# Optimization experiments

Measured on AMD Instinct MI355X. Metric: run time of the kernel, lower is better.

The kernel has to match this reference:

```python
import jax, jax.numpy as jnp
import numpy as np

B, T, N = 16, 16, 1024          # patients, max visits, code_num
C, G, H, A, P = 48, 32, 150, 32, 32  # code_size, graph_size, hidden_size, t_attention_size, pool attn size
OUT = 1
NEG = -1e30


def setup_inputs() -> dict:
    key = jax.random.key(0)
    ks = jax.random.split(key, 20)
    code_x = (jax.random.uniform(ks[0], (B, T, N)) < 0.2).astype(jnp.float32)
    neighbors = (jax.random.uniform(ks[1], (B, T, N)) < 0.2).astype(jnp.float32)
    cat = jax.random.randint(ks[2], (B, T, N), 0, 8)
    # divided[..., 0/1/2] = disjoint m1 (persistent) / m2 (emerging-neighbor) / m3 (emerging-unrelated) masks
    divided = jnp.stack([(cat == 0), (cat == 1), (cat == 2)], axis=-1).astype(jnp.int32)
    lens = jax.random.randint(ks[3], (B,), 1, T + 1)
    prior = jax.random.uniform(ks[4], (N,))
    adj = (jax.random.uniform(ks[5], (N, N)) * (jax.random.uniform(ks[6], (N, N)) < 0.05)).astype(jnp.float32)

    def nrm(k, shape, scale=0.05):
        return (jax.random.normal(k, shape) * scale).astype(jnp.float32)

    return dict(
        code_x=code_x, divided=divided, neighbors=neighbors, lens=lens, prior=prior, adj=adj,
        c_emb=nrm(ks[7], (N, C)), n_emb=nrm(ks[8], (N, C)), u_emb=nrm(ks[9], (N, G)),
        Wg=nrm(ks[10], (C, G)), bg=jnp.zeros((G,), jnp.float32),
        W_ih=nrm(ks[11], (3 * H, G)), b_ih=jnp.zeros((3 * H,), jnp.float32),
        W_hh=nrm(ks[12], (3 * H, H)), b_hh=jnp.zeros((3 * H,), jnp.float32),
        Wq=nrm(ks[13], (G, A)), bq=jnp.zeros((A,), jnp.float32),
        Wk=nrm(ks[14], (G, A)), bk=jnp.zeros((A,), jnp.float32),
        Wv=nrm(ks[15], (G, H)), bv=jnp.zeros((H,), jnp.float32),
        Wp=nrm(ks[16], (H, P)), bp=jnp.zeros((P,), jnp.float32),
        ctx=nrm(ks[17], (P,)),
        Wc=nrm(ks[18], (H, OUT)), bc=jnp.zeros((OUT,), jnp.float32),
    )


def _forward(code_x, divided, neighbors, lens, prior, adj, c_emb, n_emb, u_emb,
             Wg, bg, W_ih, b_ih, W_hh, b_hh, Wq, bq, Wk, bk, Wv, bv,
             Wp, bp, ctx, Wc, bc):
    pr = prior[:, None]                                  # [N,1] disease prior scaling of graph messages
    scale = 1.0 / jnp.sqrt(jnp.asarray(A, jnp.float32))

    def gru(x, h):
        # torch nn.GRUCell semantics; x: [B,N,G], h: [B,N,H]
        gi = jnp.einsum('bng,kg->bnk', x, W_ih) + b_ih
        gh = jnp.einsum('bnh,kh->bnk', h, W_hh) + b_hh
        ir, iz, i_n = jnp.split(gi, 3, -1)
        hr, hz, h_n = jnp.split(gh, 3, -1)
        r = jax.nn.sigmoid(ir + hr)
        z = jax.nn.sigmoid(iz + hz)
        cand = jnp.tanh(i_n + r * h_n)
        return (1.0 - z) * cand + z * h

    def step(carry, xs):
        h_prev, no_prev, t = carry
        cx, nb, dv = xs                                  # [B,N], [B,N], [B,N,3]
        c = cx[..., None]
        n = nb[..., None]
        # --- GraphLayer: adjacency message passing, prior-weighted ---
        ce = c * c_emb                                   # [B,N,C]
        ne = n * n_emb
        agg_c = jnp.einsum('mn,bnc->bmc', adj, ce) * pr
        agg_n = jnp.einsum('mn,bnc->bmc', adj, ne) * pr
        co = jax.nn.leaky_relu((ce + c * (agg_c + agg_n)) @ Wg + bg)   # [B,N,G]
        no = jax.nn.leaky_relu((ne + n * (agg_n + agg_c)) @ Wg + bg)
        # --- TransitionLayer ---
        m1 = dv[..., 0] > 0
        m2 = dv[..., 1] > 0
        m3 = dv[..., 2] > 0
        m23 = m2 | m3
        h_gru = gru(co, h_prev)                          # GRU branch for persistent codes (m1)
        # attention branch: queries = prev-step neighbor embeddings (m2) or unrelated embeddings (m3)
        qf = jnp.where(m2[..., None], no_prev, 0.0) + jnp.where(m3[..., None], u_emb, 0.0)
        q = qf @ Wq + bq
        k = co @ Wk + bk
        v = co @ Wv + bv                                 # [B,N,H]
        g = jnp.einsum('bma,bna->bmn', q, k) * scale     # scores over active m2|m3 keys only
        g = jnp.where(m23[:, None, :], g, NEG)
        h_att = jnp.tanh(jnp.einsum('bmn,bnh->bmh', jax.nn.softmax(g, axis=-1), v))
        t_pos = (t > 0).astype(co.dtype)                 # m23 branch only runs for t > 0 (as in original)
        h_new = jnp.where(m1[..., None], h_gru, 0.0) + t_pos * jnp.where(m23[..., None], h_att, 0.0)
        # masked maxes (0 when the index set is empty, as in original)
        om1 = jnp.max(jnp.where(m1[..., None], h_gru, NEG), axis=1)
        om1 = jnp.where(jnp.any(m1, axis=1)[:, None], om1, 0.0)
        om23 = jnp.max(jnp.where(m23[..., None], h_att, NEG), axis=1)
        om23 = jnp.where(jnp.any(m23, axis=1)[:, None], om23, 0.0)
        out_t = om1 + t_pos * om23                       # [B,H]
        return (h_new, no, t + 1), out_t

    h0 = jnp.zeros((B, N, H), jnp.float32)
    no0 = jnp.zeros((B, N, G), jnp.float32)
    xs = (jnp.transpose(code_x, (1, 0, 2)),
          jnp.transpose(neighbors, (1, 0, 2)),
          jnp.transpose(divided, (1, 0, 2, 3)))
    _, outs = jax.lax.scan(step, (h0, no0, jnp.int32(0)), xs)
    outs = jnp.transpose(outs, (1, 0, 2))                # [B,T,H]
    # --- DotProductAttention pooling over valid (ragged) timesteps ---
    vu = (outs @ Wp + bp) @ ctx                          # [B,T]
    valid = jnp.arange(T)[None, :] < lens[:, None]
    score = jax.nn.softmax(jnp.where(valid, vu, NEG), axis=-1)
    pooled = jnp.sum(outs * score[..., None], axis=1)    # [B,H]
    # --- Classifier (dropout identity at eval, activation=None) ---
    return pooled @ Wc + bc


def reference(code_x, divided, neighbors, lens, prior, adj, c_emb, n_emb, u_emb,
              Wg, bg, W_ih, b_ih, W_hh, b_hh, Wq, bq, Wk, bk, Wv, bv,
              Wp, bp, ctx, Wc, bc):
    return _forward(code_x, divided, neighbors, lens, prior, adj, c_emb, n_emb, u_emb,
                    Wg, bg, W_ih, b_ih, W_hh, b_hh, Wq, bq, Wk, bk, Wv, bv,
                    Wp, bp, ctx, Wc, bc)
```

## Files before the change

kernel.cpp:

```cpp
#include <hip/hip_runtime.h>

#define B_ 16
#define T_ 16
#define N_ 1024
#define C_ 48
#define G_ 32
#define H_ 150
#define A_ 32
#define P_ 32
#define H3_ 450
#define NNZ_CAP 262144
#define CAP1 256
#define CAP23 384
#define CHCAP 40960
#define CHCAPL 16384
#define SCALE_ 0.17677669529663687f

__device__ __forceinline__ unsigned fenc(float f){
  unsigned u = __float_as_uint(f);
  return (u & 0x80000000u) ? ~u : (u | 0x80000000u);
}
__device__ __forceinline__ float fdec(unsigned e){
  unsigned u = (e & 0x80000000u) ? (e & 0x7fffffffu) : ~e;
  return __uint_as_float(u);
}
__device__ __forceinline__ float sigmf(float x){ return 1.f/(1.f+__expf(-x)); }
__device__ __forceinline__ float wmaxf(float v){
  #pragma unroll
  for (int d=32; d>0; d>>=1) v = fmaxf(v, __shfl_xor(v,d));
  return v;
}

#define FMA16(W, PTR, ACC) do { \
    const float4* _c4 = (const float4*)(PTR); \
    float4 _c0=_c4[0], _c1=_c4[1], _c2=_c4[2], _c3=_c4[3]; \
    ACC[0]=fmaf((W),_c0.x,ACC[0]); ACC[1]=fmaf((W),_c0.y,ACC[1]); \
    ACC[2]=fmaf((W),_c0.z,ACC[2]); ACC[3]=fmaf((W),_c0.w,ACC[3]); \
    ACC[4]=fmaf((W),_c1.x,ACC[4]); ACC[5]=fmaf((W),_c1.y,ACC[5]); \
    ACC[6]=fmaf((W),_c1.z,ACC[6]); ACC[7]=fmaf((W),_c1.w,ACC[7]); \
    ACC[8]=fmaf((W),_c2.x,ACC[8]); ACC[9]=fmaf((W),_c2.y,ACC[9]); \
    ACC[10]=fmaf((W),_c2.z,ACC[10]); ACC[11]=fmaf((W),_c2.w,ACC[11]); \
    ACC[12]=fmaf((W),_c3.x,ACC[12]); ACC[13]=fmaf((W),_c3.y,ACC[13]); \
    ACC[14]=fmaf((W),_c3.z,ACC[14]); ACC[15]=fmaf((W),_c3.w,ACC[15]); \
  } while(0)

__global__ void k_csr_cnt(const float* __restrict__ adj, int* __restrict__ rcnt){
  int m = blockIdx.x; int tid = threadIdx.x;
  int c = 0;
  for (int n = tid; n < N_; n += 256) c += (adj[(size_t)m*N_+n] != 0.f) ? 1 : 0;
  __shared__ int sr[256];
  sr[tid]=c; __syncthreads();
  for (int s=128; s>0; s>>=1){ if (tid<s) sr[tid]+=sr[tid+s]; __syncthreads(); }
  if (tid==0) rcnt[m]=sr[0];
}
__global__ void k_csr_scan(const int* __restrict__ rcnt, int* __restrict__ rowptr){
  int lane = threadIdx.x;
  int s = 0;
  for (int r=0;r<16;++r) s += rcnt[lane*16+r];
  int incl = s;
  for (int d=1; d<64; d<<=1){ int y = __shfl_up(incl, d); if (lane>=d) incl += y; }
  int run = incl - s;
  for (int r=0;r<16;++r){ rowptr[lane*16+r] = run; run += rcnt[lane*16+r]; }
  if (lane==63) rowptr[N_] = incl;
}
__global__ void k_csr_fill(const float* __restrict__ adj, const float* __restrict__ prior,
                           const int* __restrict__ rowptr,
                           int* __restrict__ ccol, float* __restrict__ cval){
  int m = blockIdx.x; int lane = threadIdx.x;
  int base = rowptr[m];
  float pm = prior[m];
  for (int it=0; it<N_/64; ++it){
    int n = it*64+lane;
    float a = adj[(size_t)m*N_+n];
    bool pnz = (a != 0.f);
    unsigned long long mk = __ballot(pnz);
    if (pnz){
      int idx = base + __popcll(mk & ((1ULL<<lane)-1ULL));
      if (idx < NNZ_CAP){ ccol[idx]=n; cval[idx]=a*pm; }
    }
    base += __popcll(mk);
  }
}

__global__ void k_masks(const int* __restrict__ divided, int* __restrict__ lst23,
                        int* __restrict__ pos1,
                        int* __restrict__ cnt23, int* __restrict__ cnt1){
  int bt = blockIdx.x; int lane = threadIdx.x;
  int base23=0, base1=0;
  for (int it=0; it<N_/64; ++it){
    int n = it*64+lane;
    const int* dv = &divided[((size_t)bt*N_+n)*3];
    int d0=dv[0], d1=dv[1], d2=dv[2];
    bool p23 = (d1>0)||(d2>0); bool p1 = d0>0;
    unsigned long long mk23 = __ballot(p23);
    unsigned long long mk1  = __ballot(p1);
    unsigned long long ltm = (1ULL<<lane)-1ULL;
    if (p23){ int idx = base23 + __popcll(mk23 & ltm); lst23[(size_t)bt*N_+idx]=n; }
    if (p1){ int idx = base1 + __popcll(mk1 & ltm); pos1[(size_t)bt*N_+n]=idx; }
    base23 += __popcll(mk23); base1 += __popcll(mk1);
  }
  if (lane==0){ cnt23[bt]=base23; cnt1[bt]=base1; }
}

__global__ void k_chains(const int* __restrict__ divided,
                         unsigned* __restrict__ chN, int* __restrict__ nchN,
                         unsigned* __restrict__ chH, int* __restrict__ nchH,
                         unsigned* __restrict__ chL, int* __restrict__ nchL){
  int idx = blockIdx.x*256 + threadIdx.x;
  if (idx >= B_*N_) return;
  int b = idx >> 10, n = idx & (N_-1);
  unsigned m1m = 0;
  for (int t=0;t<T_;++t){
    int d0 = divided[(((size_t)(b*T_+t))*N_ + n)*3];
    if (d0>0) m1m |= (1u<<t);
  }
  unsigned heads = m1m & ~(m1m<<1);
  while (heads){
    int t0 = __builtin_ctz(heads); heads &= (heads-1u);
    unsigned run = m1m >> t0;
    int len = __builtin_ctz(~run);
    unsigned enc = ((unsigned)b<<18)|((unsigned)n<<8)|((unsigned)t0<<4)|(unsigned)(len-1);
    int f = 0;
    if (t0 >= 2){
      size_t pidx = ((size_t)(b*T_+t0-1)*N_ + n)*3;
      if ((divided[pidx+1] | divided[pidx+2]) > 0) f = 1;
    }
    if (f){ int i2 = atomicAdd(nchH,1); if (i2 < CHCAP) chH[i2]=enc; }
    else  { int i2 = atomicAdd(nchN,1); if (i2 < CHCAP) chN[i2]=enc; }
    if (len >= 2){
      int i2 = atomicAdd(nchL, 1);
      if (i2 < CHCAPL) chL[i2] = enc;
    }
  }
}

__global__ void k_wt(const float* __restrict__ W_ih, const float* __restrict__ W_hh,
                     const float* __restrict__ Wq, const float* __restrict__ bq,
                     const float* __restrict__ Wk, const float* __restrict__ Wv,
                     float* __restrict__ WihT, float* __restrict__ WhhT,
                     float* __restrict__ Md, float* __restrict__ WvT){
  int idx = blockIdx.x*256+threadIdx.x;
  if (idx < G_*H3_){ int g=idx/H3_, k=idx-g*H3_; WihT[g*H3_+k]=W_ih[(size_t)k*G_+g]; }
  int idx2 = idx - G_*H3_;
  if (idx2>=0 && idx2 < H_*H3_){ int h=idx2/H3_, k=idx2-h*H3_; WhhT[h*H3_+k]=W_hh[(size_t)k*H_+h]; }
  int e = idx - (G_*H3_ + H_*H3_);
  if (e>=0 && e<1024){
    int g=e>>5, gp=e&31;
    float acc=0.f;
    #pragma unroll
    for (int a=0;a<A_;++a) acc = fmaf(Wq[g*A_+a], Wk[gp*A_+a], acc);
    Md[e]=acc;
  }
  int e2 = e - 1024;
  if (e2>=0 && e2<32){
    float acc=0.f;
    #pragma unroll
    for (int a=0;a<A_;++a) acc = fmaf(Wk[e2*A_+a], bq[a], acc);
    Md[1024+e2]=acc;
  }
  int e3 = e - 1056;
  if (e3>=0 && e3 < H_*G_){
    int h = e3>>5, g = e3&31;
    WvT[e3] = Wv[(size_t)g*H_+h];
  }
}

__global__ void k_init(float* __restrict__ om23f, int* __restrict__ nchN,
                       int* __restrict__ nchH, int* __restrict__ nchL){
  int i = blockIdx.x*256+threadIdx.x;
  if (i<B_*T_*H_){ om23f[i]=0.f; }
  if (i==0){ *nchN = 0; *nchH = 0; *nchL = 0; }
}

__global__ __launch_bounds__(256) void k_cono(
    const float* __restrict__ code_x, const float* __restrict__ neighbors,
    const int* __restrict__ divided,
    const int* __restrict__ rowptr, const int* __restrict__ ccol, const float* __restrict__ cval,
    const float* __restrict__ c_emb, const float* __restrict__ n_emb,
    const float* __restrict__ Wg, const float* __restrict__ bg,
    float* __restrict__ co, float* __restrict__ no_)
{
  __shared__ float sCo[4][C_], sNo[4][C_];
  int w = threadIdx.x >> 6, lane = threadIdx.x & 63;
  int gw = blockIdx.x*4 + w;
  int bt = gw >> 10, m = gw & (N_-1);
  int t = bt & (T_-1);
  const int* dv = &divided[(size_t)gw*3];
  int d0=dv[0], d1=dv[1], d2=dv[2];
  bool needCo = (d0|d1|d2) > 0;
  bool needNo = (t < T_-1) && (divided[((size_t)(gw+N_))*3+1] > 0);
  if (!needCo && !needNo) return;
  float cxm = code_x[gw], nbm = neighbors[gw];
  float acc = 0.f;
  bool needAcc = (needCo && cxm!=0.f) || (needNo && nbm!=0.f);
  if (needAcc){
    int s = rowptr[m], e = rowptr[m+1];
    if (s > NNZ_CAP) s = NNZ_CAP;
    if (e > NNZ_CAP) e = NNZ_CAP;
    int btN = bt << 10;
    for (int base = s; base < e; base += 64){
      int j = base + lane;
      int cc = 0; float wx = 0.f, wy = 0.f;
      if (j < e){
        cc = ccol[j];
        float cv = cval[j];
        float xs = code_x[btN+cc], ys = neighbors[btN+cc];
        wx = cv*xs; wy = cv*ys;
      }
      unsigned long long mk = __ballot(wx!=0.f || wy!=0.f);
      while (mk){
        int u0 = __builtin_ctzll(mk); mk &= (mk-1ULL);
        int u1 = -1;
        if (mk){ u1 = __builtin_ctzll(mk); mk &= (mk-1ULL); }
        int u1s = (u1>=0)? u1 : u0;
        int n0 = __shfl(cc,u0); float a0x=__shfl(wx,u0), a0y=__shfl(wy,u0);
        int n1 = __shfl(cc,u1s); float a1x=__shfl(wx,u1s), a1y=__shfl(wy,u1s);
        float ce0=0.f,ne0=0.f,ce1=0.f,ne1=0.f;
        if (lane < C_){
          ce0 = c_emb[(size_t)n0*C_+lane]; ne0 = n_emb[(size_t)n0*C_+lane];
          ce1 = c_emb[(size_t)n1*C_+lane]; ne1 = n_emb[(size_t)n1*C_+lane];
        }
        acc = fmaf(a0x, ce0, acc); acc = fmaf(a0y, ne0, acc);
        if (u1>=0){ acc = fmaf(a1x, ce1, acc); acc = fmaf(a1y, ne1, acc); }
      }
    }
  }
  if (lane < C_){
    sCo[w][lane] = cxm * (c_emb[(size_t)m*C_+lane] + acc);
    sNo[w][lane] = nbm * (n_emb[(size_t)m*C_+lane] + acc);
  }
  asm volatile("s_waitcnt lgkmcnt(0)" ::: "memory");
  int g = lane & 31; bool isNo = lane >= 32;
  const float* src = isNo ? sNo[w] : sCo[w];
  float a2 = bg[g];
  #pragma unroll
  for (int c=0;c<C_;++c) a2 = fmaf(src[c], Wg[c*G_+g], a2);
  float r = a2 >= 0.f ? a2 : 0.01f*a2;
  if (isNo ? needNo : needCo){
    float* dst = isNo ? no_ : co;
    dst[(size_t)gw*G_ + g] = r;
  }
}

__global__ __launch_bounds__(768) void k_attn(
    const float* __restrict__ co, const float* __restrict__ no_,
    const float* __restrict__ u_emb, const int* __restrict__ divided,
    const int* __restrict__ lst23, const int* __restrict__ cnt23, const int* __restrict__ pos1,
    const float* __restrict__ Md, const float* __restrict__ WvT, const float* __restrict__ bv,
    float* __restrict__ hsel, float* __restrict__ om23f)
{
  int b = blockIdx.x; int t = blockIdx.y + 1; int bt = b*T_ + t;
  int cnt = cnt23[bt]; if (cnt > CAP23) cnt = CAP23;
  if (cnt == 0) return;
  __shared__ int   sLst[CAP23];
  __shared__ __align__(16) float sCo[CAP23][G_];
  __shared__ float sL[CAP23];
  __shared__ unsigned sMax[H_];
  int tid = threadIdx.x;
  int grp = (tid >= 384) ? 1 : 0;
  int r   = tid - 384*grp;
  unsigned sent = fenc(-1e30f);
  for (int i=tid; i<cnt; i+=768) sLst[i] = lst23[(size_t)bt*N_+i];
  for (int i=tid; i<H_; i+=768) sMax[i] = sent;
  __syncthreads();
  for (int i=tid; i<cnt*8; i+=768){
    int rrow = i>>3, seg = i&7;
    float4 v = *(const float4*)&co[((((size_t)bt<<10) + sLst[rrow])<<5) + seg*4];
    *(float4*)&sCo[rrow][seg*4] = v;
  }
  bool act = (r < cnt);
  int n = 0;
  float qpp[G_];
  if (act){
    n = sLst[r];
    int d1 = divided[((size_t)bt*N_+n)*3+1];
    const float* qsrc = (d1>0) ? &no_[((((size_t)(bt-1))<<10)+n)<<5] : &u_emb[(size_t)n*G_];
    float4 qv[8];
    #pragma unroll
    for (int j=0;j<8;++j) qv[j] = ((const float4*)qsrc)[j];
    #pragma unroll
    for (int j=0;j<G_;++j) qpp[j] = Md[1024+j];
    #pragma unroll
    for (int g=0; g<G_; ++g){
      float qfg = (g&3)==0 ? qv[g>>2].x : (g&3)==1 ? qv[g>>2].y : (g&3)==2 ? qv[g>>2].z : qv[g>>2].w;
      const float4* mr = (const float4*)&Md[g*G_];
      #pragma unroll
      for (int j=0;j<8;++j){
        float4 mj = mr[j];
        qpp[4*j+0] = fmaf(qfg, mj.x, qpp[4*j+0]);
        qpp[4*j+1] = fmaf(qfg, mj.y, qpp[4*j+1]);
        qpp[4*j+2] = fmaf(qfg, mj.z, qpp[4*j+2]);
        qpp[4*j+3] = fmaf(qfg, mj.w, qpp[4*j+3]);
      }
    }
  } else {
    #pragma unroll
    for (int j=0;j<G_;++j) qpp[j]=0.f;
  }
  __syncthreads();
  int half = (cnt+1)>>1;
  int c0 = grp ? half : 0;
  int c1 = grp ? cnt  : half;
  float pbar[G_]; float l = 0.f;
  #pragma unroll
  for (int j=0;j<G_;++j) pbar[j]=0.f;
  if (act){
    #pragma unroll 2
    for (int c=c0;c<c1;++c){
      const float4* col = (const float4*)&sCo[c][0];
      float4 xv[8];
      #pragma unroll
      for (int j=0;j<8;++j) xv[j]=col[j];
      float d0=0.f,d1v=0.f,d2v=0.f,d3=0.f;
      #pragma unroll
      for (int j=0;j<8;j+=4){
        d0 = fmaf(qpp[4*j+0], xv[j].x, d0); d1v = fmaf(qpp[4*j+1], xv[j].y, d1v);
        d2v = fmaf(qpp[4*j+2], xv[j].z, d2v); d3 = fmaf(qpp[4*j+3], xv[j].w, d3);
        d0 = fmaf(qpp[4*j+4], xv[j+1].x, d0); d1v = fmaf(qpp[4*j+5], xv[j+1].y, d1v);
        d2v = fmaf(qpp[4*j+6], xv[j+1].z, d2v); d3 = fmaf(qpp[4*j+7], xv[j+1].w, d3);
        d0 = fmaf(qpp[4*j+8], xv[j+2].x, d0); d1v = fmaf(qpp[4*j+9], xv[j+2].y, d1v);
        d2v = fmaf(qpp[4*j+10], xv[j+2].z, d2v); d3 = fmaf(qpp[4*j+11], xv[j+2].w, d3);
        d0 = fmaf(qpp[4*j+12], xv[j+3].x, d0); d1v = fmaf(qpp[4*j+13], xv[j+3].y, d1v);
        d2v = fmaf(qpp[4*j+14], xv[j+3].z, d2v); d3 = fmaf(qpp[4*j+15], xv[j+3].w, d3);
      }
      float dot = (d0+d1v)+(d2v+d3);
      float pv = __expf(dot*SCALE_);
      l += pv;
      #pragma unroll
      for (int j=0;j<8;++j){
        pbar[4*j+0] = fmaf(pv, xv[j].x, pbar[4*j+0]);
        pbar[4*j+1] = fmaf(pv, xv[j].y, pbar[4*j+1]);
        pbar[4*j+2] = fmaf(pv, xv[j].z, pbar[4*j+2]);
        pbar[4*j+3] = fmaf(pv, xv[j].w, pbar[4*j+3]);
      }
    }
  }
  __syncthreads();
  if (act && grp==0){
    #pragma unroll
    for (int j=0;j<G_;++j) sCo[r][j] = pbar[j];
    sL[r] = l;
  }
  __syncthreads();
  if (act && grp==1){
    #pragma unroll
    for (int j=0;j<G_;++j) sCo[r][j] += pbar[j];
    sL[r] += l;
  }
  __syncthreads();
  float pb[G_];
  if (act){
    float inv = 1.f / sL[r];
    const float4* pr = (const float4*)&sCo[r][0];
    #pragma unroll
    for (int j=0;j<8;++j){
      float4 pv4 = pr[j];
      pb[4*j+0]=pv4.x*inv; pb[4*j+1]=pv4.y*inv; pb[4*j+2]=pv4.z*inv; pb[4*j+3]=pv4.w*inv;
    }
  } else {
    #pragma unroll
    for (int j=0;j<G_;++j) pb[j]=0.f;
  }
  bool wsel=false; float* hd=nullptr;
  if (act && t+1 < T_){
    size_t nidx = ((size_t)b*T_+(t+1))*N_ + n;
    if (divided[nidx*3+0] > 0){
      int pos = pos1[nidx];
      if (pos >= 0 && pos < CAP1){ wsel=true; hd=&hsel[(((size_t)b*T_+t)*CAP1 + pos)*H_]; }
    }
  }
  int lane = tid & 63;
  int hA = grp*75, hB = hA + 75;
  for (int h=hA; h<hB; ++h){
    float acc = bv[h];
    const float4* wr = (const float4*)&WvT[h*G_];
    #pragma unroll
    for (int j=0;j<8;++j){
      float4 wj = wr[j];
      acc = fmaf(pb[4*j+0], wj.x, acc);
      acc = fmaf(pb[4*j+1], wj.y, acc);
      acc = fmaf(pb[4*j+2], wj.z, acc);
      acc = fmaf(pb[4*j+3], wj.w, acc);
    }
    float o = act ? tanhf(acc) : -1e30f;
    float om = wmaxf(o);
    if (lane==0) atomicMax(&sMax[h], fenc(om));
    if (wsel) hd[h] = o;
  }
  __syncthreads();
  for (int i=tid; i<H_; i+=768) om23f[(size_t)bt*H_+i] = fdec(sMax[i]);
}

__global__ __launch_bounds__(256) void k_gruheadN(
    const float* __restrict__ co, const int* __restrict__ pos1,
    const unsigned* __restrict__ chN, const int* __restrict__ nchN,
    const float* __restrict__ WihT, const float* __restrict__ b_ih,
    const float* __restrict__ b_hh, float* __restrict__ gout)
{
  __shared__ __align__(16) float sCoT[G_][16];
  __shared__ float sG[16][452];
  __shared__ int sBt[16], sN[16], sPos[16];
  int tid = threadIdx.x;
  int NC = *nchN; if (NC > CHCAP) NC = CHCAP;
  int base = blockIdx.x * 16;
  if (base >= NC) return;
  int num = min(16, NC - base);
  if (tid < 16){
    if (tid < num){
      unsigned cl = chN[base+tid];
      int b = cl>>18, n = (cl>>8)&1023, t0 = (cl>>4)&15;
      int bt = b*T_ + t0;
      sBt[tid]=bt; sN[tid]=n; sPos[tid]=pos1[(size_t)bt*N_+n];
    } else { sBt[tid]=0; sN[tid]=0; sPos[tid]=-1; }
  }
  __syncthreads();
  for (int i=tid; i<G_*16; i+=256){
    int g = i>>4, ii = i&15;
    sCoT[g][ii] = (ii<num) ? co[((size_t)sBt[ii]*N_+sN[ii])*G_+g] : 0.f;
  }
  __syncthreads();
  for (int pass=0; pass<2; ++pass){
    int k = pass*256 + tid;
    if (k < H3_){
      float acc[16];
      #pragma unroll
      for (int u=0;u<16;++u) acc[u]=0.f;
      for (int g=0; g<G_; ++g){
        float wih = WihT[g*H3_ + k];
        FMA16(wih, &sCoT[g][0], acc);
      }
      #pragma unroll
      for (int u=0;u<16;++u) sG[u][k] = acc[u];
    }
  }
  __syncthreads();
  for (int i=tid; i<num*152; i+=256){
    int s = i/152, h = i - s*152;
    if (h < H_){
      int pos = sPos[s];
      if (pos >= 0 && pos < CAP1){
        float r = sigmf(sG[s][h]       + b_ih[h]       + b_hh[h]);
        float z = sigmf(sG[s][h+H_]    + b_ih[h+H_]    + b_hh[h+H_]);
        float cand = tanhf(sG[s][h+2*H_] + b_ih[h+2*H_] + r*b_hh[h+2*H_]);
        gout[((size_t)sBt[s]*CAP1 + pos)*H_ + h] = (1.f-z)*cand;
      }
    }
  }
}

__global__ __launch_bounds__(256) void k_gruheadH(
    const float* __restrict__ co, const float* __restrict__ hsel,
    const int* __restrict__ pos1,
    const unsigned* __restrict__ chH, const int* __restrict__ nchH,
    const float* __restrict__ WihT, const float* __restrict__ b_ih,
    const float* __restrict__ WhhT, const float* __restrict__ b_hh,
    float* __restrict__ gout)
{
  __shared__ __align__(16) float sCoT[G_][16];
  __shared__ __align__(16) float sHT[152][16];
  __shared__ float sG[16][452];
  __shared__ float sGhn[16][152];
  __shared__ int sBt[16], sN[16], sPos[16], sHo[16];
  int tid = threadIdx.x;
  int NC = *nchH; if (NC > CHCAP) NC = CHCAP;
  int base = blockIdx.x * 16;
  if (base >= NC) return;
  int num = min(16, NC - base);
  if (tid < 16){
    if (tid < num){
      unsigned cl = chH[base+tid];
      int b = cl>>18, n = (cl>>8)&1023, t0 = (cl>>4)&15;
      int bt = b*T_ + t0;
      int pos = pos1[(size_t)bt*N_+n];
      sBt[tid]=bt; sN[tid]=n; sPos[tid]=pos;
      sHo[tid] = (b*T_ + (t0-1))*CAP1 + ((pos>=0 && pos<CAP1) ? pos : 0);
    } else { sBt[tid]=0; sN[tid]=0; sPos[tid]=-1; sHo[tid]=0; }
  }
  __syncthreads();
  for (int i=tid; i<G_*16; i+=256){
    int g = i>>4, ii = i&15;
    sCoT[g][ii] = (ii<num) ? co[((size_t)sBt[ii]*N_+sN[ii])*G_+g] : 0.f;
  }
  for (int i=tid; i<152*16; i+=256){
    int q = i>>4, ii = i&15;
    float v = 0.f;
    if (ii < num && q < H_) v = hsel[(size_t)sHo[ii]*H_ + q];
    sHT[q][ii] = v;
  }
  __syncthreads();
  for (int pass=0; pass<2; ++pass){
    int k = pass*256 + tid;
    if (k < H3_){
      float acc[16];
      #pragma unroll
      for (int u=0;u<16;++u) acc[u]=0.f;
      for (int g=0; g<G_; ++g){
        float wih = WihT[g*H3_ + k];
        FMA16(wih, &sCoT[g][0], acc);
      }
      #pragma unroll
      for (int u=0;u<16;++u) sG[u][k] = acc[u];
    }
  }
  for (int pass=0; pass<2; ++pass){
    int k = pass*256 + tid;
    if (k < H3_){
      float acc[16];
      #pragma unroll
      for (int u=0;u<16;++u) acc[u]=0.f;
      for (int q=0; q<H_; ++q){
        float whh = WhhT[q*H3_ + k];
        FMA16(whh, &sHT[q][0], acc);
      }
      if (k < 2*H_){
        #pragma unroll
        for (int u=0;u<16;++u) sG[u][k] += acc[u];
      } else {
        #pragma unroll
        for (int u=0;u<16;++u) sGhn[u][k-2*H_] = acc[u];
      }
    }
  }
  __syncthreads();
  for (int i=tid; i<num*152; i+=256){
    int s = i/152, h = i - s*152;
    if (h < H_){
      int pos = sPos[s];
      if (pos >= 0 && pos < CAP1){
        float hv = sHT[h][s];
        float r = sigmf(sG[s][h]       + b_ih[h]       + b_hh[h]);
        float z = sigmf(sG[s][h+H_]    + b_ih[h+H_]    + b_hh[h+H_]);
        float cand = tanhf(sG[s][h+2*H_] + b_ih[h+2*H_] + r*(sGhn[s][h] + b_hh[h+2*H_]));
        float o = (1.f-z)*cand + z*hv;
        gout[((size_t)sBt[s]*CAP1 + pos)*H_ + h] = o;
      }
    }
  }
}

__global__ __launch_bounds__(256) void k_grutail(
    const float* __restrict__ co, const int* __restrict__ pos1,
    const unsigned* __restrict__ chainsL, const int* __restrict__ nchL,
    const float* __restrict__ WihT, const float* __restrict__ b_ih,
    const float* __restrict__ WhhT, const float* __restrict__ b_hh,
    float* __restrict__ gout)
{
  __shared__ float hst[4][4][H_];
  int w = threadIdx.x >> 6, lane = threadIdx.x & 63;
  int NC = *nchL; if (NC > CHCAPL) NC = CHCAPL;
  int cbase = (blockIdx.x*4 + w)*4;
  if (cbase >= NC) return;

  int cbv[4], cnv[4], t0v[4], lenv[4];
  #pragma unroll
  for (int u=0;u<4;++u){
    int cid = cbase+u; bool ca = cid < NC;
    unsigned cl = chainsL[ca ? cid : (NC-1)];
    cbv[u]=cl>>18; cnv[u]=(cl>>8)&1023; t0v[u]=(cl>>4)&15;
    lenv[u]= ca ? (int)((cl&15)+1) : 1;
  }
  int maxlen = lenv[0];
  #pragma unroll
  for (int u=1;u<4;++u) maxlen = max(maxlen, lenv[u]);

  int h0=lane,h1=lane+64,h2=lane+128; bool has2=(h2<H_); int h2c=has2?h2:0;
  float bi[9], bh[9];
  bi[0]=b_ih[h0]; bi[1]=b_ih[h0+H_]; bi[2]=b_ih[h0+2*H_];
  bi[3]=b_ih[h1]; bi[4]=b_ih[h1+H_]; bi[5]=b_ih[h1+2*H_];
  bi[6]=b_ih[h2c]; bi[7]=b_ih[h2c+H_]; bi[8]=b_ih[h2c+2*H_];
  bh[0]=b_hh[h0]; bh[1]=b_hh[h0+H_]; bh[2]=b_hh[h0+2*H_];
  bh[3]=b_hh[h1]; bh[4]=b_hh[h1+H_]; bh[5]=b_hh[h1+2*H_];
  bh[6]=b_hh[h2c]; bh[7]=b_hh[h2c+H_]; bh[8]=b_hh[h2c+2*H_];

  for (int s=1; s<maxlen; ++s){
    bool as[4]; int btv[4];
    const float* hp[4];
    #pragma unroll
    for (int u=0;u<4;++u){
      as[u] = s < lenv[u];
      int t = t0v[u] + (as[u] ? s : 0);
      btv[u] = cbv[u]*T_ + t;
      if (s == 1 && as[u]){
        int btp = btv[u] - 1;
        int posp = pos1[(size_t)btp*N_ + cnv[u]];
        if (posp < 0 || posp >= CAP1) posp = 0;
        hp[u] = &gout[((size_t)btp*CAP1 + posp)*H_];
      } else {
        hp[u] = &hst[w][u][0];
      }
    }
    float gi[4][9], gh[4][9];
    #pragma unroll
    for (int u=0;u<4;++u){
      #pragma unroll
      for (int j=0;j<9;++j){ gi[u][j]=bi[j]; gh[u][j]=bh[j]; }
    }
    const float* cop[4];
    #pragma unroll
    for (int u=0;u<4;++u) cop[u] = &co[((size_t)btv[u]*N_ + cnv[u])*G_];
    for (int g=0; g<G_; ++g){
      const float* wr = &WihT[g*H3_];
      float wv[9];
      wv[0]=wr[h0]; wv[1]=wr[h0+H_]; wv[2]=wr[h0+2*H_];
      wv[3]=wr[h1]; wv[4]=wr[h1+H_]; wv[5]=wr[h1+2*H_];
      wv[6]=wr[h2c]; wv[7]=wr[h2c+H_]; wv[8]=wr[h2c+2*H_];
      #pragma unroll
      for (int u=0;u<4;++u){
        float cg = cop[u][g];
        #pragma unroll
        for (int j=0;j<9;++j) gi[u][j]=fmaf(cg, wv[j], gi[u][j]);
      }
    }
    for (int q=0;q<H_;++q){
      const float* wr=&WhhT[q*H3_];
      float wv[9];
      wv[0]=wr[h0]; wv[1]=wr[h0+H_]; wv[2]=wr[h0+2*H_];
      wv[3]=wr[h1]; wv[4]=wr[h1+H_]; wv[5]=wr[h1+2*H_];
      wv[6]=wr[h2c]; wv[7]=wr[h2c+H_]; wv[8]=wr[h2c+2*H_];
      #pragma unroll
      for (int u=0;u<4;++u){
        float hv = hp[u][q];
        #pragma unroll
        for (int j=0;j<9;++j) gh[u][j]=fmaf(hv, wv[j], gh[u][j]);
      }
    }
    #pragma unroll
    for (int u=0;u<4;++u){
      if (as[u]){
        float hv0 = hp[u][h0];
        float hv1 = hp[u][h1];
        float hv2 = has2 ? hp[u][h2] : 0.f;
        float r0=sigmf(gi[u][0]+gh[u][0]), z0=sigmf(gi[u][1]+gh[u][1]);
        float cd0=tanhf(gi[u][2]+r0*gh[u][2]);
        float o0=(1.f-z0)*cd0 + z0*hv0;
        float r1=sigmf(gi[u][3]+gh[u][3]), z1=sigmf(gi[u][4]+gh[u][4]);
        float cd1=tanhf(gi[u][5]+r1*gh[u][5]);
        float o1=(1.f-z1)*cd1 + z1*hv1;
        float o2=0.f;
        if (has2){
          float r2=sigmf(gi[u][6]+gh[u][6]), z2=sigmf(gi[u][7]+gh[u][7]);
          float cd2=tanhf(gi[u][8]+r2*gh[u][8]);
          o2=(1.f-z2)*cd2 + z2*hv2;
        }
        float* hd = &hst[w][u][0];
        hd[h0]=o0; hd[h1]=o1; if (has2) hd[h2]=o2;
        int pos = pos1[(size_t)btv[u]*N_ + cnv[u]];
        if (pos >= 0 && pos < CAP1){
          float* gd = &gout[((size_t)btv[u]*CAP1 + pos)*H_];
          gd[h0]=o0; gd[h1]=o1; if (has2) gd[h2]=o2;
        }
      }
    }
    asm volatile("s_waitcnt lgkmcnt(0)" ::: "memory");
  }
}

__global__ __launch_bounds__(256) void k_om1(
    const float* __restrict__ gout, const int* __restrict__ cnt1, float* __restrict__ om1f)
{
  int bt = blockIdx.x; int tid = threadIdx.x;
  int c1 = cnt1[bt]; if (c1 > CAP1) c1 = CAP1;
  if (tid < H_){
    float mx = -1e30f;
    for (int r=0;r<c1;++r) mx = fmaxf(mx, gout[((size_t)bt*CAP1+r)*H_+tid]);
    om1f[(size_t)bt*H_+tid] = (c1>0) ? mx : 0.f;
  }
}

__global__ __launch_bounds__(256) void k_final(
    const float* __restrict__ om1f, const float* __restrict__ om23f,
    const float* __restrict__ Wp, const float* __restrict__ bp,
    const float* __restrict__ ctx, const float* __restrict__ Wc, const float* __restrict__ bc,
    const int* __restrict__ lens, float* __restrict__ out)
{
  int b = blockIdx.x; int tid = threadIdx.x;
  __shared__ float sOut[T_][H_];
  __shared__ float sTP[T_][P_];
  __shared__ float sVu[T_], sSc[T_], sPool[H_];
  __shared__ float sRed[256];
  for (int i=tid; i<T_*H_; i+=256){
    int t=i/H_, h=i-t*H_;
    float o1 = om1f[((size_t)b*T_+t)*H_+h];
    float o2 = (t>0)? om23f[((size_t)b*T_+t)*H_+h] : 0.f;
    sOut[t][h]=o1+o2;
  }
  __syncthreads();
  for (int pr = tid; pr < T_*P_; pr += 256){
    int t = pr / P_, p = pr - t*P_;
    float acc = bp[p];
    for (int h=0;h<H_;++h) acc = fmaf(sOut[t][h], Wp[h*P_+p], acc);
    sTP[t][p] = acc * ctx[p];
  }
  __syncthreads();
  if (tid < T_){
    float v=0.f;
    for (int p=0;p<P_;++p) v += sTP[tid][p];
    sVu[tid]=v;
  }
  __syncthreads();
  if (tid==0){
    int L = lens[b]; if (L<1) L=1; if (L>T_) L=T_;
    float mx=-1e30f;
    for (int t=0;t<L;++t) mx = fmaxf(mx, sVu[t]);
    float s=0.f;
    for (int t=0;t<L;++t){ float e=__expf(sVu[t]-mx); sSc[t]=e; s+=e; }
    float inv=1.f/s;
    for (int t=0;t<T_;++t) sSc[t] = (t<L)? sSc[t]*inv : 0.f;
  }
  __syncthreads();
  if (tid < H_){
    float acc=0.f;
    for (int t=0;t<T_;++t) acc = fmaf(sOut[t][tid], sSc[t], acc);
    sPool[tid]=acc;
  }
  __syncthreads();
  float v = (tid<H_)? sPool[tid]*Wc[tid] : 0.f;
  sRed[tid]=v; __syncthreads();
  for (int s=128;s>0;s>>=1){ if (tid<s) sRed[tid]+=sRed[tid+s]; __syncthreads(); }
  if (tid==0) out[b] = sRed[0] + bc[0];
}

extern "C" void kernel_launch(void* const* d_in, const int* in_sizes, int n_in,
                              void* d_out, int out_size, void* d_ws, size_t ws_size,
                              hipStream_t stream)
{
  const float* code_x=(const float*)d_in[0];
  const int*   divided=(const int*)d_in[1];
  const float* neighbors=(const float*)d_in[2];
  const int*   lens=(const int*)d_in[3];
  const float* prior=(const float*)d_in[4];
  const float* adj=(const float*)d_in[5];
  const float* c_emb=(const float*)d_in[6];
  const float* n_emb=(const float*)d_in[7];
  const float* u_emb=(const float*)d_in[8];
  const float* Wg=(const float*)d_in[9];
  const float* bg=(const float*)d_in[10];
  const float* W_ih=(const float*)d_in[11];
  const float* b_ih=(const float*)d_in[12];
  const float* W_hh=(const float*)d_in[13];
  const float* b_hh=(const float*)d_in[14];
  const float* Wq=(const float*)d_in[15];
  const float* bq=(const float*)d_in[16];
  const float* Wk=(const float*)d_in[17];
  const float* bk=(const float*)d_in[18];
  const float* Wv=(const float*)d_in[19];
  const float* bv=(const float*)d_in[20];
  const float* Wp=(const float*)d_in[21];
  const float* bp=(const float*)d_in[22];
  const float* ctx=(const float*)d_in[23];
  const float* Wc=(const float*)d_in[24];
  const float* bc=(const float*)d_in[25];
  float* out=(float*)d_out;
  (void)in_sizes; (void)n_in; (void)out_size; (void)ws_size; (void)bk;

  char* p=(char*)d_ws;
  size_t off=0;
  auto carve=[&](size_t bytes)->char*{ char* r=p+off; off=(off+bytes+255)&~(size_t)255; return r; };
  int*   rowptr=(int*)carve((N_+1)*4);
  int*   rcnt  =(int*)carve(N_*4);
  int*   ccol  =(int*)carve((size_t)NNZ_CAP*4);
  float* cval  =(float*)carve((size_t)NNZ_CAP*4);
  int*   cnt23 =(int*)carve(B_*T_*4);
  int*   cnt1  =(int*)carve(B_*T_*4);
  int*   lst23 =(int*)carve((size_t)B_*T_*N_*4);
  int*   pos1  =(int*)carve((size_t)B_*T_*N_*4);
  float* co    =(float*)carve((size_t)B_*T_*N_*G_*4);
  float* no_   =(float*)carve((size_t)B_*T_*N_*G_*4);
  float* WihT  =(float*)carve((size_t)G_*H3_*4);
  float* WhhT  =(float*)carve((size_t)H_*H3_*4);
  float* Md    =(float*)carve(1056*4);
  float* WvT   =(float*)carve((size_t)H_*G_*4);
  float* hsel  =(float*)carve((size_t)B_*T_*CAP1*H_*4);
  float* gout  =(float*)carve((size_t)B_*T_*CAP1*H_*4);
  unsigned* chainsN=(unsigned*)carve((size_t)CHCAP*4);
  unsigned* chainsH=(unsigned*)carve((size_t)CHCAP*4);
  unsigned* chainsL=(unsigned*)carve((size_t)CHCAPL*4);
  int*   nchN  =(int*)carve(256);
  int*   nchH  =(int*)carve(256);
  int*   nchL  =(int*)carve(256);
  float* om1f  =(float*)carve((size_t)B_*T_*H_*4);
  float* om23f =(float*)carve((size_t)B_*T_*H_*4);

  k_csr_cnt<<<N_,256,0,stream>>>(adj, rcnt);
  k_csr_scan<<<1,64,0,stream>>>(rcnt, rowptr);
  k_csr_fill<<<N_,64,0,stream>>>(adj, prior, rowptr, ccol, cval);
  k_masks<<<B_*T_,64,0,stream>>>(divided, lst23, pos1, cnt23, cnt1);
  k_wt<<<343,256,0,stream>>>(W_ih, W_hh, Wq, bq, Wk, Wv, WihT, WhhT, Md, WvT);
  k_init<<<(B_*T_*H_+255)/256,256,0,stream>>>(om23f, nchN, nchH, nchL);
  k_chains<<<(B_*N_+255)/256,256,0,stream>>>(divided, chainsN, nchN, chainsH, nchH, chainsL, nchL);
  k_cono<<<B_*T_*N_/4,256,0,stream>>>(code_x, neighbors, divided, rowptr, ccol, cval,
                                      c_emb, n_emb, Wg, bg, co, no_);
  k_attn<<<dim3(B_, T_-1),768,0,stream>>>(co, no_, u_emb, divided,
                                      lst23, cnt23, pos1, Md, WvT, bv,
                                      hsel, om23f);
  k_gruheadN<<<CHCAP/16,256,0,stream>>>(co, pos1, chainsN, nchN,
                                      WihT, b_ih, b_hh, gout);
  k_gruheadH<<<CHCAP/16,256,0,stream>>>(co, hsel, pos1, chainsH, nchH,
                                      WihT, b_ih, WhhT, b_hh, gout);
  k_grutail<<<CHCAPL/16,256,0,stream>>>(co, pos1, chainsL, nchL,
                                      WihT, b_ih, WhhT, b_hh, gout);
  k_om1<<<B_*T_,256,0,stream>>>(gout, cnt1, om1f);
  k_final<<<B_,256,0,stream>>>(om1f, om23f, Wp,bp,ctx,Wc,bc, lens, out);
}
```

Measured before the change: 479.0 us.

## Split attention over two key halves and batch GRU tail steps by level

The attention kernel is split into a partial pass and a combine pass. The partial pass runs two blocks per (b,t), each handling half of the key set and writing partial sums to global memory, and the combine pass merges them and applies the value projection. The sequential chain-tail GRU is replaced by level-wise batched kernels that process step 1 and step 2 of all chains in 16-wide tiles using shared-memory transposes. A small per-lane kernel handles only chains longer than three. This exposes more parallelism in both stages at the cost of extra launches, global scratch traffic, and fixed capacity limits (8192/2048/256) that could overflow.

Measured after the change: 517.0 us. 7.9% more time.

```diff
diff --git a/kernel.cpp b/kernel.cpp
--- a/kernel.cpp
+++ b/kernel.cpp
@@ -13,7 +13,7 @@
 #define CAP1 256
 #define CAP23 384
 #define CHCAP 40960
-#define CHCAPL 16384
+#define DCAP 256
 #define SCALE_ 0.17677669529663687f
 
 __device__ __forceinline__ unsigned fenc(float f){
@@ -105,7 +105,8 @@
 __global__ void k_chains(const int* __restrict__ divided,
                          unsigned* __restrict__ chN, int* __restrict__ nchN,
                          unsigned* __restrict__ chH, int* __restrict__ nchH,
-                         unsigned* __restrict__ chL, int* __restrict__ nchL){
+                         unsigned* __restrict__ chLv, int* __restrict__ nLv,
+                         unsigned* __restrict__ chD){
   int idx = blockIdx.x*256 + threadIdx.x;
   if (idx >= B_*N_) return;
   int b = idx >> 10, n = idx & (N_-1);
@@ -127,10 +128,9 @@
     }
     if (f){ int i2 = atomicAdd(nchH,1); if (i2 < CHCAP) chH[i2]=enc; }
     else  { int i2 = atomicAdd(nchN,1); if (i2 < CHCAP) chN[i2]=enc; }
-    if (len >= 2){
-      int i2 = atomicAdd(nchL, 1);
-      if (i2 < CHCAPL) chL[i2] = enc;
-    }
+    if (len >= 2){ int i2 = atomicAdd(&nLv[1],1); if (i2 < 8192) chLv[i2]=enc; }
+    if (len >= 3){ int i2 = atomicAdd(&nLv[2],1); if (i2 < 2048) chLv[8192+i2]=enc; }
+    if (len >= 4){ int i2 = atomicAdd(&nLv[3],1); if (i2 < DCAP) chD[i2]=enc; }
   }
 }
 
@@ -166,10 +166,11 @@
 }
 
 __global__ void k_init(float* __restrict__ om23f, int* __restrict__ nchN,
-                       int* __restrict__ nchH, int* __restrict__ nchL){
+                       int* __restrict__ nchH, int* __restrict__ nLv){
   int i = blockIdx.x*256+threadIdx.x;
   if (i<B_*T_*H_){ om23f[i]=0.f; }
-  if (i==0){ *nchN = 0; *nchH = 0; *nchL = 0; }
+  if (i==0){ *nchN = 0; *nchH = 0; }
+  if (i<16) nLv[i]=0;
 }
 
 __global__ __launch_bounds__(256) void k_cono(
@@ -242,37 +243,49 @@
   }
 }
 
-__global__ __launch_bounds__(768) void k_attn(
+__global__ __launch_bounds__(768) void k_attnP(
     const float* __restrict__ co, const float* __restrict__ no_,
     const float* __restrict__ u_emb, const int* __restrict__ divided,
-    const int* __restrict__ lst23, const int* __restrict__ cnt23, const int* __restrict__ pos1,
-    const float* __restrict__ Md, const float* __restrict__ WvT, const float* __restrict__ bv,
-    float* __restrict__ hsel, float* __restrict__ om23f)
+    const int* __restrict__ lst23, const int* __restrict__ cnt23,
+    const float* __restrict__ Md,
+    float* __restrict__ pbH, float* __restrict__ lH)
 {
   int b = blockIdx.x; int t = blockIdx.y + 1; int bt = b*T_ + t;
+  int z = blockIdx.z;
+  int idx = b*(T_-1) + (t-1);
   int cnt = cnt23[bt]; if (cnt > CAP23) cnt = CAP23;
   if (cnt == 0) return;
-  __shared__ int   sLst[CAP23];
-  __shared__ __align__(16) float sCo[CAP23][G_];
-  __shared__ float sL[CAP23];
-  __shared__ unsigned sMax[H_];
   int tid = threadIdx.x;
   int grp = (tid >= 384) ? 1 : 0;
   int r   = tid - 384*grp;
-  unsigned sent = fenc(-1e30f);
-  for (int i=tid; i<cnt; i+=768) sLst[i] = lst23[(size_t)bt*N_+i];
-  for (int i=tid; i<H_; i+=768) sMax[i] = sent;
-  __syncthreads();
-  for (int i=tid; i<cnt*8; i+=768){
-    int rrow = i>>3, seg = i&7;
-    float4 v = *(const float4*)&co[((((size_t)bt<<10) + sLst[rrow])<<5) + seg*4];
-    *(float4*)&sCo[rrow][seg*4] = v;
+  float* pbOut = &pbH[(size_t)(z*B_*(T_-1) + idx)*CAP23*G_];
+  float* lOut  = &lH[(size_t)(z*B_*(T_-1) + idx)*CAP23];
+  int half = (cnt+1)>>1;
+  int cs = z*half;
+  int ce = cs + half; if (ce > cnt) ce = cnt;
+  int hc = ce - cs;
+  if (hc <= 0){
+    if (tid < cnt){
+      for (int j=0;j<G_;++j) pbOut[(size_t)tid*G_+j]=0.f;
+      lOut[tid]=0.f;
+    }
+    return;
+  }
+  __shared__ int sLstH[192];
+  __shared__ __align__(16) float sCo[192][G_];
+  __shared__ float sPb[CAP23][G_];
+  __shared__ float sL[CAP23];
+  for (int i=tid; i<hc; i+=768) sLstH[i] = lst23[(size_t)bt*N_ + cs + i];
+  __syncthreads();
+  for (int i=tid; i<hc*8; i+=768){
+    int c = i>>3, seg = i&7;
+    float4 v = *(const float4*)&co[((((size_t)bt<<10) + sLstH[c])<<5) + seg*4];
+    *(float4*)&sCo[c][seg*4] = v;
   }
   bool act = (r < cnt);
-  int n = 0;
   float qpp[G_];
   if (act){
-    n = sLst[r];
+    int n = lst23[(size_t)bt*N_ + r];
     int d1 = divided[((size_t)bt*N_+n)*3+1];
     const float* qsrc = (d1>0) ? &no_[((((size_t)(bt-1))<<10)+n)<<5] : &u_emb[(size_t)n*G_];
     float4 qv[8];
@@ -298,9 +311,9 @@
     for (int j=0;j<G_;++j) qpp[j]=0.f;
   }
   __syncthreads();
-  int half = (cnt+1)>>1;
-  int c0 = grp ? half : 0;
-  int c1 = grp ? cnt  : half;
+  int hh = (hc+1)>>1;
+  int c0 = grp ? hh : 0;
+  int c1 = grp ? hc : hh;
   float pbar[G_]; float l = 0.f;
   #pragma unroll
   for (int j=0;j<G_;++j) pbar[j]=0.f;
@@ -338,24 +351,54 @@
   __syncthreads();
   if (act && grp==0){
     #pragma unroll
-    for (int j=0;j<G_;++j) sCo[r][j] = pbar[j];
+    for (int j=0;j<G_;++j) sPb[r][(j+r)&31] = pbar[j];
     sL[r] = l;
   }
   __syncthreads();
   if (act && grp==1){
     #pragma unroll
-    for (int j=0;j<G_;++j) sCo[r][j] += pbar[j];
+    for (int j=0;j<G_;++j) sPb[r][(j+r)&31] += pbar[j];
     sL[r] += l;
   }
   __syncthreads();
+  for (int i=tid; i<cnt*G_; i+=768){
+    int rr = i>>5, j = i&31;
+    pbOut[(size_t)rr*G_ + j] = sPb[rr][(j+rr)&31];
+  }
+  for (int i=tid; i<cnt; i+=768) lOut[i] = sL[i];
+}
+
+__global__ __launch_bounds__(768) void k_attnC(
+    const int* __restrict__ divided, const int* __restrict__ lst23,
+    const int* __restrict__ cnt23, const int* __restrict__ pos1,
+    const float* __restrict__ WvT, const float* __restrict__ bv,
+    const float* __restrict__ pbH, const float* __restrict__ lH,
+    float* __restrict__ hsel, float* __restrict__ om23f)
+{
+  int b = blockIdx.x; int t = blockIdx.y + 1; int bt = b*T_ + t;
+  int idx = b*(T_-1) + (t-1);
+  int cnt = cnt23[bt]; if (cnt > CAP23) cnt = CAP23;
+  if (cnt == 0) return;
+  __shared__ unsigned sMax[H_];
+  int tid = threadIdx.x;
+  int grp = (tid >= 384) ? 1 : 0;
+  int r   = tid - 384*grp;
+  int lane = tid & 63;
+  unsigned sent = fenc(-1e30f);
+  for (int i=tid; i<H_; i+=768) sMax[i] = sent;
+  __syncthreads();
+  bool act = (r < cnt);
   float pb[G_];
   if (act){
-    float inv = 1.f / sL[r];
-    const float4* pr = (const float4*)&sCo[r][0];
+    const float4* p0 = (const float4*)&pbH[((size_t)(0*B_*(T_-1) + idx)*CAP23 + r)*G_];
+    const float4* p1 = (const float4*)&pbH[((size_t)(1*B_*(T_-1) + idx)*CAP23 + r)*G_];
+    float l = lH[(size_t)(0*B_*(T_-1)+idx)*CAP23 + r] + lH[(size_t)(1*B_*(T_-1)+idx)*CAP23 + r];
+    float inv = 1.f/l;
     #pragma unroll
     for (int j=0;j<8;++j){
-      float4 pv4 = pr[j];
-      pb[4*j+0]=pv4.x*inv; pb[4*j+1]=pv4.y*inv; pb[4*j+2]=pv4.z*inv; pb[4*j+3]=pv4.w*inv;
+      float4 a = p0[j], c = p1[j];
+      pb[4*j+0]=(a.x+c.x)*inv; pb[4*j+1]=(a.y+c.y)*inv;
+      pb[4*j+2]=(a.z+c.z)*inv; pb[4*j+3]=(a.w+c.w)*inv;
     }
   } else {
     #pragma unroll
@@ -363,13 +406,13 @@
   }
   bool wsel=false; float* hd=nullptr;
   if (act && t+1 < T_){
+    int n = lst23[(size_t)bt*N_ + r];
     size_t nidx = ((size_t)b*T_+(t+1))*N_ + n;
     if (divided[nidx*3+0] > 0){
       int pos = pos1[nidx];
       if (pos >= 0 && pos < CAP1){ wsel=true; hd=&hsel[(((size_t)b*T_+t)*CAP1 + pos)*H_]; }
     }
   }
-  int lane = tid & 63;
   int hA = grp*75, hB = hA + 75;
   for (int h=hA; h<hB; ++h){
     float acc = bv[h];
@@ -538,16 +581,108 @@
   }
 }
 
-__global__ __launch_bounds__(256) void k_grutail(
+__global__ __launch_bounds__(256) void k_grulev(
     const float* __restrict__ co, const int* __restrict__ pos1,
-    const unsigned* __restrict__ chainsL, const int* __restrict__ nchL,
+    const unsigned* __restrict__ chLv, const int* __restrict__ nLv,
+    const float* __restrict__ WihT, const float* __restrict__ b_ih,
+    const float* __restrict__ WhhT, const float* __restrict__ b_hh,
+    float* __restrict__ gout, int s, int cap)
+{
+  __shared__ __align__(16) float sCoT[G_][16];
+  __shared__ __align__(16) float sHT[152][16];
+  __shared__ float sG[16][452];
+  __shared__ float sGhn[16][152];
+  __shared__ int sBt[16], sN[16], sPos[16], sHo[16];
+  int tid = threadIdx.x;
+  int NC = *nLv; if (NC > cap) NC = cap;
+  int base = blockIdx.x * 16;
+  if (base >= NC) return;
+  int num = min(16, NC - base);
+  if (tid < 16){
+    if (tid < num){
+      unsigned cl = chLv[base+tid];
+      int b = cl>>18, n = (cl>>8)&1023, t0 = (cl>>4)&15;
+      int bt = b*T_ + t0 + s;
+      int pos = pos1[(size_t)bt*N_+n];
+      int posp = pos1[(size_t)(bt-1)*N_+n];
+      if (posp < 0 || posp >= CAP1) posp = 0;
+      sBt[tid]=bt; sN[tid]=n; sPos[tid]=pos;
+      sHo[tid] = (bt-1)*CAP1 + posp;
+    } else { sBt[tid]=0; sN[tid]=0; sPos[tid]=-1; sHo[tid]=0; }
+  }
+  __syncthreads();
+  for (int i=tid; i<G_*16; i+=256){
+    int g = i>>4, ii = i&15;
+    sCoT[g][ii] = (ii<num) ? co[((size_t)sBt[ii]*N_+sN[ii])*G_+g] : 0.f;
+  }
+  for (int i=tid; i<152*16; i+=256){
+    int q = i>>4, ii = i&15;
+    float v = 0.f;
+    if (ii < num && q < H_) v = gout[(size_t)sHo[ii]*H_ + q];
+    sHT[q][ii] = v;
+  }
+  __syncthreads();
+  for (int pass=0; pass<2; ++pass){
+    int k = pass*256 + tid;
+    if (k < H3_){
+      float acc[16];
+      #pragma unroll
+      for (int u=0;u<16;++u) acc[u]=0.f;
+      for (int g=0; g<G_; ++g){
+        float wih = WihT[g*H3_ + k];
+        FMA16(wih, &sCoT[g][0], acc);
+      }
+      #pragma unroll
+      for (int u=0;u<16;++u) sG[u][k] = acc[u];
+    }
+  }
+  for (int pass=0; pass<2; ++pass){
+    int k = pass*256 + tid;
+    if (k < H3_){
+      float acc[16];
+      #pragma unroll
+      for (int u=0;u<16;++u) acc[u]=0.f;
+      for (int q=0; q<H_; ++q){
+        float whh = WhhT[q*H3_ + k];
+        FMA16(whh, &sHT[q][0], acc);
+      }
+      if (k < 2*H_){
+        #pragma unroll
+        for (int u=0;u<16;++u) sG[u][k] += acc[u];
+      } else {
+        #pragma unroll
+        for (int u=0;u<16;++u) sGhn[u][k-2*H_] = acc[u];
+      }
+    }
+  }
+  __syncthreads();
+  for (int i=tid; i<num*152; i+=256){
+    int sl = i/152, h = i - sl*152;
+    if (h < H_){
+      int pos = sPos[sl];
+      if (pos >= 0 && pos < CAP1){
+        float hv = sHT[h][sl];
+        float r = sigmf(sG[sl][h]       + b_ih[h]       + b_hh[h]);
+        float z = sigmf(sG[sl][h+H_]    + b_ih[h+H_]    + b_hh[h+H_]);
+        float cand = tanhf(sG[sl][h+2*H_] + b_ih[h+2*H_] + r*(sGhn[sl][h] + b_hh[h+2*H_]));
+        float o = (1.f-z)*cand + z*hv;
+        gout[((size_t)sBt[sl]*CAP1 + pos)*H_ + h] = o;
+      }
+    }
+  }
+}
+
+__global__ __launch_bounds__(256) void k_grudeep(
+    const float* __restrict__ co, const int* __restrict__ pos1,
+    const unsigned* __restrict__ chD, const int* __restrict__ nD,
     const float* __restrict__ WihT, const float* __restrict__ b_ih,
     const float* __restrict__ WhhT, const float* __restrict__ b_hh,
     float* __restrict__ gout)
 {
   __shared__ float hst[4][4][H_];
   int w = threadIdx.x >> 6, lane = threadIdx.x & 63;
-  int NC = *nchL; if (NC > CHCAPL) NC = CHCAPL;
+  int NC = *nD; if (NC > DCAP) NC = DCAP;
+  if (NC == 0) return;
   int cbase = (blockIdx.x*4 + w)*4;
   if (cbase >= NC) return;
 
@@ -555,9 +690,9 @@
   #pragma unroll
   for (int u=0;u<4;++u){
     int cid = cbase+u; bool ca = cid < NC;
-    unsigned cl = chainsL[ca ? cid : (NC-1)];
+    unsigned cl = chD[ca ? cid : (NC-1)];
     cbv[u]=cl>>18; cnv[u]=(cl>>8)&1023; t0v[u]=(cl>>4)&15;
-    lenv[u]= ca ? (int)((cl&15)+1) : 1;
+    lenv[u]= ca ? (int)((cl&15)+1) : 3;
   }
   int maxlen = lenv[0];
   #pragma unroll
@@ -572,7 +707,7 @@
   bh[3]=b_hh[h1]; bh[4]=b_hh[h1+H_]; bh[5]=b_hh[h1+2*H_];
   bh[6]=b_hh[h2c]; bh[7]=b_hh[h2c+H_]; bh[8]=b_hh[h2c+2*H_];
 
-  for (int s=1; s<maxlen; ++s){
+  for (int s=3; s<maxlen; ++s){
     bool as[4]; int btv[4];
     const float* hp[4];
     #pragma unroll
@@ -580,7 +715,7 @@
       as[u] = s < lenv[u];
       int t = t0v[u] + (as[u] ? s : 0);
       btv[u] = cbv[u]*T_ + t;
-      if (s == 1 && as[u]){
+      if (s == 3 && as[u]){
         int btp = btv[u] - 1;
         int posp = pos1[(size_t)btp*N_ + cnv[u]];
         if (posp < 0 || posp >= CAP1) posp = 0;
@@ -772,12 +907,15 @@
   float* WvT   =(float*)carve((size_t)H_*G_*4);
   float* hsel  =(float*)carve((size_t)B_*T_*CAP1*H_*4);
   float* gout  =(float*)carve((size_t)B_*T_*CAP1*H_*4);
+  float* pbH   =(float*)carve((size_t)2*B_*(T_-1)*CAP23*G_*4);
+  float* lH    =(float*)carve((size_t)2*B_*(T_-1)*CAP23*4);
   unsigned* chainsN=(unsigned*)carve((size_t)CHCAP*4);
   unsigned* chainsH=(unsigned*)carve((size_t)CHCAP*4);
-  unsigned* chainsL=(unsigned*)carve((size_t)CHCAPL*4);
+  unsigned* chLv  =(unsigned*)carve((size_t)10240*4);
+  unsigned* chD   =(unsigned*)carve((size_t)DCAP*4);
   int*   nchN  =(int*)carve(256);
   int*   nchH  =(int*)carve(256);
-  int*   nchL  =(int*)carve(256);
+  int*   nLv   =(int*)carve(256);
   float* om1f  =(float*)carve((size_t)B_*T_*H_*4);
   float* om23f =(float*)carve((size_t)B_*T_*H_*4);
 
@@ -786,18 +924,23 @@
   k_csr_fill<<<N_,64,0,stream>>>(adj, prior, rowptr, ccol, cval);
   k_masks<<<B_*T_,64,0,stream>>>(divided, lst23, pos1, cnt23, cnt1);
   k_wt<<<343,256,0,stream>>>(W_ih, W_hh, Wq, bq, Wk, Wv, WihT, WhhT, Md, WvT);
-  k_init<<<(B_*T_*H_+255)/256,256,0,stream>>>(om23f, nchN, nchH, nchL);
-  k_chains<<<(B_*N_+255)/256,256,0,stream>>>(divided, chainsN, nchN, chainsH, nchH, chainsL, nchL);
+  k_init<<<(B_*T_*H_+255)/256,256,0,stream>>>(om23f, nchN, nchH, nLv);
+  k_chains<<<(B_*N_+255)/256,256,0,stream>>>(divided, chainsN, nchN, chainsH, nchH, chLv, nLv, chD);
   k_cono<<<B_*T_*N_/4,256,0,stream>>>(code_x, neighbors, divided, rowptr, ccol, cval,
                                       c_emb, n_emb, Wg, bg, co, no_);
-  k_attn<<<dim3(B_, T_-1),768,0,stream>>>(co, no_, u_emb, divided,
-                                      lst23, cnt23, pos1, Md, WvT, bv,
-                                      hsel, om23f);
+  k_attnP<<<dim3(B_, T_-1, 2),768,0,stream>>>(co, no_, u_emb, divided,
+                                      lst23, cnt23, Md, pbH, lH);
+  k_attnC<<<dim3(B_, T_-1),768,0,stream>>>(divided, lst23, cnt23, pos1,
+                                      WvT, bv, pbH, lH, hsel, om23f);
   k_gruheadN<<<CHCAP/16,256,0,stream>>>(co, pos1, chainsN, nchN,
                                       WihT, b_ih, b_hh, gout);
   k_gruheadH<<<CHCAP/16,256,0,stream>>>(co, hsel, pos1, chainsH, nchH,
                                       WihT, b_ih, WhhT, b_hh, gout);
-  k_grutail<<<CHCAPL/16,256,0,stream>>>(co, pos1, chainsL, nchL,
+  k_grulev<<<512,256,0,stream>>>(co, pos1, chLv, nLv+1,
+                                      WihT, b_ih, WhhT, b_hh, gout, 1, 8192);
+  k_grulev<<<128,256,0,stream>>>(co, pos1, chLv+8192, nLv+2,
+                                      WihT, b_ih, WhhT, b_hh, gout, 2, 2048);
+  k_grudeep<<<DCAP/16,256,0,stream>>>(co, pos1, chD, nLv+3,
                                       WihT, b_ih, WhhT, b_hh, gout);
   k_om1<<<B_*T_,256,0,stream>>>(gout, cnt1, om1f);
   k_final<<<B_,256,0,stream>>>(om1f, om23f, Wp,bp,ctx,Wc,bc, lens, out);
```
